# Optimization experiments

Measured on AMD Instinct MI355X. Metric: run time of the kernel, lower is better.

The kernel has to match this reference:

```python
import jax, jax.numpy as jnp
import numpy as np

H, W = 72, 128            # raster_h, raster_w
THICK = 0.03              # raster_thickness
SHARP = 80.0              # sigmoid sharpness
NRS = 64                  # match_resample_n
BIG = 1e9                 # finite stand-in for inf (grad-safe)
PTS_W, TAN_W, CURV_W, OVL_W = 5.0, 1.0, 0.5, 2.0


def _grid_xy():
    ys = jnp.linspace(0.0, 1.0, H)
    xs = jnp.linspace(0.0, 1.0, W)
    yy, xx = jnp.meshgrid(ys, xs, indexing='ij')
    return jnp.stack([xx, yy], -1).reshape(-1, 2)  # [H*W, 2]


def _prepare_mask(vis):
    # visibility -> per-point mask; curves with <2 visible points fall back to all-visible
    raw = vis > 0.5
    fallback = raw.sum(-1) < 2
    return jnp.where(fallback[:, None], 1.0, raw.astype(jnp.float32))  # [m, p]


def _resample(curves, pm, num):
    # arc-length resampling of [m, p, 2] polylines to [m, num, 2]
    m, p, _ = curves.shape
    seg_valid = pm[:, :-1] * pm[:, 1:]
    seg_len = jnp.linalg.norm(curves[:, 1:] - curves[:, :-1], axis=-1) * seg_valid
    cum = jnp.concatenate([jnp.zeros((m, 1), curves.dtype), jnp.cumsum(seg_len, -1)], -1)  # [m, p]
    total = cum[:, -1]
    base_t = jnp.linspace(0.0, 1.0, num)
    t = base_t[None] * total[:, None]  # [m, num]
    idx = jax.vmap(lambda c, tt: jnp.searchsorted(c, tt, side='right'))(cum, t) - 1
    idx = jnp.clip(idx, 0, p - 2)
    left = jnp.take_along_axis(curves[:, :-1], idx[..., None], axis=1)
    right = jnp.take_along_axis(curves[:, 1:], idx[..., None], axis=1)
    lt = jnp.take_along_axis(cum[:, :-1], idx, axis=1)
    rt = jnp.take_along_axis(cum[:, 1:], idx, axis=1)
    alpha = ((t - lt) / jnp.maximum(rt - lt, 1e-8))[..., None]
    out = left + alpha * (right - left)
    return jnp.where((total < 1e-8)[:, None, None], curves[:, :1, :], out)


def _tangents(pts):
    # central-difference unit tangents, [m, n, 2]
    fwd = jnp.concatenate([pts[:, 1:2] - pts[:, 0:1],
                           pts[:, 2:] - pts[:, :-2],
                           pts[:, -1:] - pts[:, -2:-1]], axis=1)
    return fwd / jnp.maximum(jnp.linalg.norm(fwd, axis=-1, keepdims=True), 1e-8)


def _pt2poly(A, B):
    # mean over resampled points of A of min point-to-segment distance to polyline B
    # A: [qa, r, 2], B: [qb, r, 2] -> [qa, qb]
    seg_a = B[:, :-1]
    ab = B[:, 1:] - seg_a
    denom = jnp.maximum((ab * ab).sum(-1), 1e-8)  # [qb, s]
    ap = A[:, None, :, None, :] - seg_a[None, :, None]           # [qa, qb, r, s, 2]
    t = jnp.clip((ap * ab[None, :, None]).sum(-1) / denom[None, :, None], 0.0, 1.0)
    proj = seg_a[None, :, None] + t[..., None] * ab[None, :, None]
    dist = jnp.linalg.norm(A[:, None, :, None, :] - proj, axis=-1)  # [qa, qb, r, s]
    return dist.min(-1).mean(-1)


def _smooth_l1(x, y):
    d = jnp.abs(x - y)
    return jnp.where(d < 1.0, 0.5 * d * d, d - 0.5)


def _soft_mask(curves, pm, grid):
    # soft rasterization of polylines: [m, p, 2] -> [m, H*W]
    seg_a = curves[:, :-1]
    ab = curves[:, 1:] - seg_a
    denom = jnp.maximum((ab * ab).sum(-1), 1e-8)          # [m, s]
    seg_valid = (pm[:, :-1] * pm[:, 1:]) > 0.5
    ap = grid[None, :, None, :] - seg_a[:, None]          # [m, HW, s, 2]
    t = jnp.clip((ap * ab[:, None]).sum(-1) / denom[:, None], 0.0, 1.0)
    proj = seg_a[:, None] + t[..., None] * ab[:, None]
    dist = jnp.linalg.norm(grid[None, :, None, :] - proj, axis=-1)  # [m, HW, s]
    dist = jnp.where(seg_valid[:, None], dist, BIG)
    min_dist = dist.min(-1)
    # fallback to nearest visible point when a curve has no valid segment
    no_valid = ~seg_valid.any(-1)
    pd = jnp.linalg.norm(grid[None, :, None, :] - curves[:, None], axis=-1)  # [m, HW, p]
    pd = jnp.where(pm[:, None] > 0.5, pd, BIG)
    min_dist = jnp.where(no_valid[:, None], pd.min(-1), min_dist)
    return jax.nn.sigmoid((THICK - min_dist) * SHARP)


def _cost_single(pred, gtp, gtv, grid):
    gt_pm = _prepare_mask(gtv)
    ones_pm = jnp.ones(pred.shape[:2], pred.dtype)
    pred_rs = _resample(pred, ones_pm, NRS)
    gt_rs = _resample(gtp, gt_pm, NRS)
    d_pg = _pt2poly(pred_rs, gt_rs)
    d_gp = _pt2poly(gt_rs, pred_rs).T
    sym = 0.5 * (d_pg + d_gp)                                   # [Q, M]
    pt = _tangents(pred_rs)
    gt_t = _tangents(gt_rs)
    tan = 1.0 - jnp.abs((pt[:, None] * gt_t[None]).sum(-1)).mean(-1)
    ps = pred_rs[:, 2:] - 2 * pred_rs[:, 1:-1] + pred_rs[:, :-2]
    gs = gt_rs[:, 2:] - 2 * gt_rs[:, 1:-1] + gt_rs[:, :-2]
    curv = _smooth_l1(ps[:, None], gs[None]).mean((-1, -2))
    pmask = _soft_mask(pred, ones_pm, grid)                     # [Q, HW]
    gmask = _soft_mask(gtp, gt_pm, grid)                        # [M, HW]
    inter = jnp.minimum(pmask[:, None], gmask[None]).sum(-1)
    union = jnp.maximum(pmask[:, None], gmask[None]).sum(-1)
    overlap = 1.0 - inter / (union + 1e-8)
    return PTS_W * sym + TAN_W * tan + CURV_W * curv + OVL_W * overlap


def setup_inputs() -> dict:
    key = jax.random.key(0)
    k1, k2, k3, k4 = jax.random.split(key, 4)
    return {
        'pred_pts': jax.random.uniform(k1, (2, 40, 24, 2), jnp.float32),
        'gt_pts': jax.random.uniform(k2, (2, 24, 24, 2), jnp.float32),
        'gt_vis': jax.random.uniform(k3, (2, 24, 24), jnp.float32),
        'gt_exist': jax.random.uniform(k4, (2, 24), jnp.float32),
    }


def reference(pred_pts, gt_pts, gt_vis, gt_exist):
    grid = _grid_xy()
    cost = jax.vmap(lambda p, g, v: _cost_single(p, g, v, grid))(pred_pts, gt_pts, gt_vis)
    # zero out columns for non-existent GT lanes (original skips them via boolean indexing)
    return cost * (gt_exist > 0.5).astype(cost.dtype)[:, None, :]  # [B, Q, M]
```

## Files before the change

### kernel.cpp

```cpp
#include <hip/hip_runtime.h>
#include <math.h>

#define Hh 72
#define Ww 128
#define HW (Hh*Ww)
#define NP 24
#define Mp 40
#define Ng 24
#define Bb 2
#define NRS 64
#define THICKc 0.03f
#define SHARPc 80.0f

__global__ __launch_bounds__(64) void k_resample(
    const float* __restrict__ pred,
    const float* __restrict__ gt,
    const float* __restrict__ vis,
    float* __restrict__ predRS,
    float* __restrict__ gtRS,
    float* __restrict__ gtPM)
{
    int blk = blockIdx.x;
    int b = blk / (Mp + Ng);
    int c = blk % (Mp + Ng);
    bool isPred = (c < Mp);
    int tid = threadIdx.x;

    __shared__ float qx[NP], qy[NP], pm[NP], cum[NP];
    __shared__ float s_total;

    const float* src = isPred ? pred + (size_t)(b * Mp + c) * NP * 2
                              : gt   + (size_t)(b * Ng + (c - Mp)) * NP * 2;
    if (tid < NP) {
        qx[tid] = src[tid * 2 + 0];
        qy[tid] = src[tid * 2 + 1];
        pm[tid] = isPred ? 1.0f
                         : ((vis[(b * Ng + (c - Mp)) * NP + tid] > 0.5f) ? 1.0f : 0.0f);
    }
    __syncthreads();
    if (tid == 0) {
        if (!isPred) {
            float s = 0.0f;
            for (int p = 0; p < NP; p++) s += pm[p];
            if (s < 2.0f)
                for (int p = 0; p < NP; p++) pm[p] = 1.0f;
        }
        float acc = 0.0f;
        cum[0] = 0.0f;
        for (int s = 0; s < NP - 1; s++) {
            float dx = qx[s + 1] - qx[s], dy = qy[s + 1] - qy[s];
            float sl = sqrtf(dx * dx + dy * dy) * (pm[s] * pm[s + 1]);
            acc += sl;
            cum[s + 1] = acc;
        }
        s_total = acc;
    }
    __syncthreads();
    if (!isPred && tid < NP) gtPM[(b * Ng + (c - Mp)) * NP + tid] = pm[tid];

    float total = s_total;
    float t = ((float)tid / 63.0f) * total;
    int cnt = 0;
    for (int p = 0; p < NP; p++) cnt += (cum[p] <= t) ? 1 : 0;
    int idx = cnt - 1;
    idx = (idx < 0) ? 0 : ((idx > NP - 2) ? NP - 2 : idx);
    float lt = cum[idx], rt = cum[idx + 1];
    float alpha = (t - lt) / fmaxf(rt - lt, 1e-8f);
    float ox = qx[idx] + alpha * (qx[idx + 1] - qx[idx]);
    float oy = qy[idx] + alpha * (qy[idx + 1] - qy[idx]);
    if (total < 1e-8f) { ox = qx[0]; oy = qy[0]; }
    float* dst = isPred ? predRS + (size_t)(b * Mp + c) * NRS * 2
                        : gtRS   + (size_t)(b * Ng + (c - Mp)) * NRS * 2;
    dst[tid * 2 + 0] = ox;
    dst[tid * 2 + 1] = oy;
}

__global__ __launch_bounds__(256) void k_softmask(
    const float* __restrict__ pred,
    const float* __restrict__ gt,
    const float* __restrict__ gtPM,
    float* __restrict__ pmask,
    float* __restrict__ gmask)
{
    int c = blockIdx.y;
    int b = c / (Mp + Ng);
    int cc = c % (Mp + Ng);
    bool isPred = (cc < Mp);
    int g = blockIdx.x * blockDim.x + threadIdx.x;

    __shared__ float qx[NP], qy[NP], pm[NP];
    if (threadIdx.x < NP) {
        const float* src = isPred ? pred + (size_t)(b * Mp + cc) * NP * 2
                                  : gt   + (size_t)(b * Ng + (cc - Mp)) * NP * 2;
        qx[threadIdx.x] = src[threadIdx.x * 2 + 0];
        qy[threadIdx.x] = src[threadIdx.x * 2 + 1];
        pm[threadIdx.x] = isPred ? 1.0f : gtPM[(b * Ng + (cc - Mp)) * NP + threadIdx.x];
    }
    __syncthreads();

    float gx = (float)(g % Ww) * (1.0f / 127.0f);
    float gy = (float)(g / Ww) * (1.0f / 71.0f);

    float best2 = 1e30f;
    bool anyValid = false;
    for (int s = 0; s < NP - 1; s++) {
        if (pm[s] * pm[s + 1] > 0.5f) {
            anyValid = true;
            float ax = qx[s], ay = qy[s];
            float abx = qx[s + 1] - ax, aby = qy[s + 1] - ay;
            float denom = fmaxf(abx * abx + aby * aby, 1e-8f);
            float t = ((gx - ax) * abx + (gy - ay) * aby) / denom;
            t = fminf(fmaxf(t, 0.0f), 1.0f);
            float dx = gx - (ax + t * abx), dy = gy - (ay + t * aby);
            best2 = fminf(best2, dx * dx + dy * dy);
        }
    }
    float mind;
    if (anyValid) {
        mind = sqrtf(best2);
    } else {
        float b2 = 1e30f;
        for (int p = 0; p < NP; p++) {
            if (pm[p] > 0.5f) {
                float dx = gx - qx[p], dy = gy - qy[p];
                b2 = fminf(b2, dx * dx + dy * dy);
            }
        }
        mind = sqrtf(b2);
    }
    float x = (THICKc - mind) * SHARPc;
    float mval = 1.0f / (1.0f + expf(-x));
    if (isPred) pmask[(size_t)(b * Mp + cc) * HW + g] = mval;
    else        gmask[(size_t)(b * Ng + (cc - Mp)) * HW + g] = mval;
}

__device__ __forceinline__ float block_reduce_sum(float v, float* red, int tid) {
    red[tid] = v;
    __syncthreads();
    for (int s = 128; s > 0; s >>= 1) {
        if (tid < s) red[tid] += red[tid + s];
        __syncthreads();
    }
    float r = red[0];
    __syncthreads();
    return r;
}

__global__ __launch_bounds__(256) void k_cost(
    const float* __restrict__ predRS,
    const float* __restrict__ gtRS,
    const float* __restrict__ pmask,
    const float* __restrict__ gmask,
    const float* __restrict__ gtExist,
    float* __restrict__ out)
{
    int pair = blockIdx.x;
    int j = pair % Ng;
    int i = (pair / Ng) % Mp;
    int b = pair / (Ng * Mp);
    int tid = threadIdx.x;

    __shared__ float px[NRS], py[NRS], gxr[NRS], gyr[NRS];
    __shared__ float red[256];

    if (tid < NRS) {
        px[tid]  = predRS[((size_t)(b * Mp + i) * NRS + tid) * 2 + 0];
        py[tid]  = predRS[((size_t)(b * Mp + i) * NRS + tid) * 2 + 1];
        gxr[tid] = gtRS[((size_t)(b * Ng + j) * NRS + tid) * 2 + 0];
        gyr[tid] = gtRS[((size_t)(b * Ng + j) * NRS + tid) * 2 + 1];
    }
    __syncthreads();

    const float* pmk = pmask + (size_t)(b * Mp + i) * HW;
    const float* gmk = gmask + (size_t)(b * Ng + j) * HW;
    float smin = 0.0f, smax = 0.0f;
    for (int g = tid; g < HW; g += 256) {
        float p = pmk[g], q = gmk[g];
        smin += fminf(p, q);
        smax += fmaxf(p, q);
    }

    float symv = 0.0f, tanv = 0.0f, curvv = 0.0f;
    if (tid < NRS) {
        float p0x = px[tid], p0y = py[tid];
        float bst = 1e30f;
        for (int s = 0; s < NRS - 1; s++) {
            float ax = gxr[s], ay = gyr[s];
            float abx = gxr[s + 1] - ax, aby = gyr[s + 1] - ay;
            float denom = fmaxf(abx * abx + aby * aby, 1e-8f);
            float t = ((p0x - ax) * abx + (p0y - ay) * aby) / denom;
            t = fminf(fmaxf(t, 0.0f), 1.0f);
            float dx = p0x - (ax + t * abx), dy = p0y - (ay + t * aby);
            bst = fminf(bst, dx * dx + dy * dy);
        }
        float dpg = sqrtf(bst);
        float q0x = gxr[tid], q0y = gyr[tid];
        bst = 1e30f;
        for (int s = 0; s < NRS - 1; s++) {
            float ax = px[s], ay = py[s];
            float abx = px[s + 1] - ax, aby = py[s + 1] - ay;
            float denom = fmaxf(abx * abx + aby * aby, 1e-8f);
            float t = ((q0x - ax) * abx + (q0y - ay) * aby) / denom;
            t = fminf(fmaxf(t, 0.0f), 1.0f);
            float dx = q0x - (ax + t * abx), dy = q0y - (ay + t * aby);
            bst = fminf(bst, dx * dx + dy * dy);
        }
        float dgp = sqrtf(bst);
        symv = 0.5f * (dpg + dgp);

        int kp = (tid == NRS - 1) ? NRS - 1 : tid + 1;
        int km = (tid == 0) ? 0 : tid - 1;
        float tx = px[kp] - px[km], ty = py[kp] - py[km];
        float nrm = fmaxf(sqrtf(tx * tx + ty * ty), 1e-8f);
        tx /= nrm; ty /= nrm;
        float gtx = gxr[kp] - gxr[km], gty = gyr[kp] - gyr[km];
        float nrm2 = fmaxf(sqrtf(gtx * gtx + gty * gty), 1e-8f);
        gtx /= nrm2; gty /= nrm2;
        tanv = fabsf(tx * gtx + ty * gty);

        if (tid < NRS - 2) {
            float psx = px[tid + 2] - 2.0f * px[tid + 1] + px[tid];
            float psy = py[tid + 2] - 2.0f * py[tid + 1] + py[tid];
            float gsx = gxr[tid + 2] - 2.0f * gxr[tid + 1] + gxr[tid];
            float gsy = gyr[tid + 2] - 2.0f * gyr[tid + 1] + gyr[tid];
            float d1 = fabsf(psx - gsx);
            float d2 = fabsf(psy - gsy);
            float c1 = (d1 < 1.0f) ? 0.5f * d1 * d1 : d1 - 0.5f;
            float c2 = (d2 < 1.0f) ? 0.5f * d2 * d2 : d2 - 0.5f;
            curvv = c1 + c2;
        }
    }

    float Smin  = block_reduce_sum(smin,  red, tid);
    float Smax  = block_reduce_sum(smax,  red, tid);
    float Ssym  = block_reduce_sum(symv,  red, tid);
    float Stan  = block_reduce_sum(tanv,  red, tid);
    float Scurv = block_reduce_sum(curvv, red, tid);

    if (tid == 0) {
        float overlap = 1.0f - Smin / (Smax + 1e-8f);
        float sym  = Ssym * (1.0f / 64.0f);
        float tanl = 1.0f - Stan * (1.0f / 64.0f);
        float curv = Scurv * (1.0f / 124.0f);
        float cost = 5.0f * sym + 1.0f * tanl + 0.5f * curv + 2.0f * overlap;
        float e = (gtExist[b * Ng + j] > 0.5f) ? 1.0f : 0.0f;
        out[(size_t)(b * Mp + i) * Ng + j] = cost * e;
    }
}

extern "C" void kernel_launch(void* const* d_in, const int* in_sizes, int n_in,
                              void* d_out, int out_size, void* d_ws, size_t ws_size,
                              hipStream_t stream) {
    (void)in_sizes; (void)n_in; (void)out_size; (void)ws_size;
    const float* pred  = (const float*)d_in[0];
    const float* gt    = (const float*)d_in[1];
    const float* vis   = (const float*)d_in[2];
    const float* exist = (const float*)d_in[3];

    float* ws     = (float*)d_ws;
    float* predRS = ws;
    float* gtRS   = predRS + (size_t)Bb * Mp * NRS * 2;
    float* gtPM   = gtRS   + (size_t)Bb * Ng * NRS * 2;
    float* pmask  = gtPM   + (size_t)Bb * Ng * NP;
    float* gmask  = pmask  + (size_t)Bb * Mp * HW;
    float* outp   = (float*)d_out;

    hipLaunchKernelGGL(k_resample, dim3(Bb * (Mp + Ng)), dim3(64), 0, stream,
                       pred, gt, vis, predRS, gtRS, gtPM);
    hipLaunchKernelGGL(k_softmask, dim3(HW / 256, Bb * (Mp + Ng)), dim3(256), 0, stream,
                       pred, gt, gtPM, pmask, gmask);
    hipLaunchKernelGGL(k_cost, dim3(Bb * Mp * Ng), dim3(256), 0, stream,
                       predRS, gtRS, pmask, gmask, exist, outp);
}
```

Measured before the change: 115.8 us.

## Derive mask union from per-mask sums and use wave-shuffle reductions

The soft-mask kernel now accumulates a per-mask total with a wave shuffle and an atomicAdd into a small buffer that the resample kernel zeroes. The cost kernel then gets the union sum as sum(p)+sum(q)-sum(min) and only computes the min term, reading through float4 loads. The five shared-memory tree reductions, each with many barriers, become wave shuffles plus one barrier. __expf and bit ops replace expf and div/mod. The cost is atomics in the mask kernel and slightly different float rounding in the union sum.

Result: slower. 167.2 us (+44.4%).

```diff
diff --git a/kernel.cpp b/kernel.cpp
--- a/kernel.cpp
+++ b/kernel.cpp
@@ -11,6 +11,7 @@
 #define NRS 64
 #define THICKc 0.03f
 #define SHARPc 80.0f
+#define NSUM (Bb*(Mp+Ng))
 
 __global__ __launch_bounds__(64) void k_resample(
     const float* __restrict__ pred,
@@ -18,13 +19,16 @@
     const float* __restrict__ vis,
     float* __restrict__ predRS,
     float* __restrict__ gtRS,
-    float* __restrict__ gtPM)
+    float* __restrict__ gtPM,
+    float* __restrict__ maskSum)
 {
     int blk = blockIdx.x;
     int b = blk / (Mp + Ng);
     int c = blk % (Mp + Ng);
     bool isPred = (c < Mp);
     int tid = threadIdx.x;
+
+    if (tid == 0) maskSum[blk] = 0.0f;
 
     __shared__ float qx[NP], qy[NP], pm[NP], cum[NP];
     __shared__ float s_total;
@@ -80,7 +84,8 @@
     const float* __restrict__ gt,
     const float* __restrict__ gtPM,
     float* __restrict__ pmask,
-    float* __restrict__ gmask)
+    float* __restrict__ gmask,
+    float* __restrict__ maskSum)
 {
     int c = blockIdx.y;
     int b = c / (Mp + Ng);
@@ -98,8 +103,8 @@
     }
     __syncthreads();
 
-    float gx = (float)(g % Ww) * (1.0f / 127.0f);
-    float gy = (float)(g / Ww) * (1.0f / 71.0f);
+    float gx = (float)(g & (Ww - 1)) * (1.0f / 127.0f);
+    float gy = (float)(g >> 7) * (1.0f / 71.0f);
 
     float best2 = 1e30f;
     bool anyValid = false;
@@ -129,21 +134,18 @@
         mind = sqrtf(b2);
     }
     float x = (THICKc - mind) * SHARPc;
-    float mval = 1.0f / (1.0f + expf(-x));
-    if (isPred) pmask[(size_t)(b * Mp + cc) * HW + g] = mval;
-    else        gmask[(size_t)(b * Ng + (cc - Mp)) * HW + g] = mval;
-}
-
-__device__ __forceinline__ float block_reduce_sum(float v, float* red, int tid) {
-    red[tid] = v;
-    __syncthreads();
-    for (int s = 128; s > 0; s >>= 1) {
-        if (tid < s) red[tid] += red[tid + s];
-        __syncthreads();
-    }
-    float r = red[0];
-    __syncthreads();
-    return r;
+    float mval = 1.0f / (1.0f + __expf(-x));
+    int sumIdx;
+    if (isPred) {
+        pmask[(size_t)(b * Mp + cc) * HW + g] = mval;
+        sumIdx = b * Mp + cc;
+    } else {
+        gmask[(size_t)(b * Ng + (cc - Mp)) * HW + g] = mval;
+        sumIdx = Bb * Mp + b * Ng + (cc - Mp);
+    }
+    float ws = mval;
+    for (int off = 32; off > 0; off >>= 1) ws += __shfl_down(ws, off);
+    if ((threadIdx.x & 63) == 0) atomicAdd(&maskSum[sumIdx], ws);
 }
 
 __global__ __launch_bounds__(256) void k_cost(
@@ -151,6 +153,7 @@
     const float* __restrict__ gtRS,
     const float* __restrict__ pmask,
     const float* __restrict__ gmask,
+    const float* __restrict__ maskSum,
     const float* __restrict__ gtExist,
     float* __restrict__ out)
 {
@@ -159,9 +162,10 @@
     int i = (pair / Ng) % Mp;
     int b = pair / (Ng * Mp);
     int tid = threadIdx.x;
+    int lane = tid & 63, wid = tid >> 6;
 
     __shared__ float px[NRS], py[NRS], gxr[NRS], gyr[NRS];
-    __shared__ float red[256];
+    __shared__ float partial[4];
 
     if (tid < NRS) {
         px[tid]  = predRS[((size_t)(b * Mp + i) * NRS + tid) * 2 + 0];
@@ -171,18 +175,17 @@
     }
     __syncthreads();
 
-    const float* pmk = pmask + (size_t)(b * Mp + i) * HW;
-    const float* gmk = gmask + (size_t)(b * Ng + j) * HW;
-    float smin = 0.0f, smax = 0.0f;
-    for (int g = tid; g < HW; g += 256) {
-        float p = pmk[g], q = gmk[g];
-        smin += fminf(p, q);
-        smax += fmaxf(p, q);
+    const float4* pm4 = (const float4*)(pmask + (size_t)(b * Mp + i) * HW);
+    const float4* gm4 = (const float4*)(gmask + (size_t)(b * Ng + j) * HW);
+    float smin = 0.0f;
+    for (int g = tid; g < HW / 4; g += 256) {
+        float4 p = pm4[g], q = gm4[g];
+        smin += fminf(p.x, q.x) + fminf(p.y, q.y) + fminf(p.z, q.z) + fminf(p.w, q.w);
     }
 
     float symv = 0.0f, tanv = 0.0f, curvv = 0.0f;
-    if (tid < NRS) {
-        float p0x = px[tid], p0y = py[tid];
+    if (wid == 0) {
+        float p0x = px[lane], p0y = py[lane];
         float bst = 1e30f;
         for (int s = 0; s < NRS - 1; s++) {
             float ax = gxr[s], ay = gyr[s];
@@ -194,7 +197,7 @@
             bst = fminf(bst, dx * dx + dy * dy);
         }
         float dpg = sqrtf(bst);
-        float q0x = gxr[tid], q0y = gyr[tid];
+        float q0x = gxr[lane], q0y = gyr[lane];
         bst = 1e30f;
         for (int s = 0; s < NRS - 1; s++) {
             float ax = px[s], ay = py[s];
@@ -208,8 +211,8 @@
         float dgp = sqrtf(bst);
         symv = 0.5f * (dpg + dgp);
 
-        int kp = (tid == NRS - 1) ? NRS - 1 : tid + 1;
-        int km = (tid == 0) ? 0 : tid - 1;
+        int kp = (lane == NRS - 1) ? NRS - 1 : lane + 1;
+        int km = (lane == 0) ? 0 : lane - 1;
         float tx = px[kp] - px[km], ty = py[kp] - py[km];
         float nrm = fmaxf(sqrtf(tx * tx + ty * ty), 1e-8f);
         tx /= nrm; ty /= nrm;
@@ -218,11 +221,11 @@
         gtx /= nrm2; gty /= nrm2;
         tanv = fabsf(tx * gtx + ty * gty);
 
-        if (tid < NRS - 2) {
-            float psx = px[tid + 2] - 2.0f * px[tid + 1] + px[tid];
-            float psy = py[tid + 2] - 2.0f * py[tid + 1] + py[tid];
-            float gsx = gxr[tid + 2] - 2.0f * gxr[tid + 1] + gxr[tid];
-            float gsy = gyr[tid + 2] - 2.0f * gyr[tid + 1] + gyr[tid];
+        if (lane < NRS - 2) {
+            float psx = px[lane + 2] - 2.0f * px[lane + 1] + px[lane];
+            float psy = py[lane + 2] - 2.0f * py[lane + 1] + py[lane];
+            float gsx = gxr[lane + 2] - 2.0f * gxr[lane + 1] + gxr[lane];
+            float gsy = gyr[lane + 2] - 2.0f * gyr[lane + 1] + gyr[lane];
             float d1 = fabsf(psx - gsx);
             float d2 = fabsf(psy - gsy);
             float c1 = (d1 < 1.0f) ? 0.5f * d1 * d1 : d1 - 0.5f;
@@ -231,17 +234,26 @@
         }
     }
 
-    float Smin  = block_reduce_sum(smin,  red, tid);
-    float Smax  = block_reduce_sum(smax,  red, tid);
-    float Ssym  = block_reduce_sum(symv,  red, tid);
-    float Stan  = block_reduce_sum(tanv,  red, tid);
-    float Scurv = block_reduce_sum(curvv, red, tid);
+    for (int off = 32; off > 0; off >>= 1) smin += __shfl_down(smin, off);
+    if (lane == 0) partial[wid] = smin;
+    if (wid == 0) {
+        for (int off = 32; off > 0; off >>= 1) {
+            symv  += __shfl_down(symv,  off);
+            tanv  += __shfl_down(tanv,  off);
+            curvv += __shfl_down(curvv, off);
+        }
+    }
+    __syncthreads();
 
     if (tid == 0) {
+        float Smin = partial[0] + partial[1] + partial[2] + partial[3];
+        float Sp = maskSum[b * Mp + i];
+        float Sq = maskSum[Bb * Mp + b * Ng + j];
+        float Smax = Sp + Sq - Smin;
         float overlap = 1.0f - Smin / (Smax + 1e-8f);
-        float sym  = Ssym * (1.0f / 64.0f);
-        float tanl = 1.0f - Stan * (1.0f / 64.0f);
-        float curv = Scurv * (1.0f / 124.0f);
+        float sym  = symv * (1.0f / 64.0f);
+        float tanl = 1.0f - tanv * (1.0f / 64.0f);
+        float curv = curvv * (1.0f / 124.0f);
         float cost = 5.0f * sym + 1.0f * tanl + 0.5f * curv + 2.0f * overlap;
         float e = (gtExist[b * Ng + j] > 0.5f) ? 1.0f : 0.0f;
         out[(size_t)(b * Mp + i) * Ng + j] = cost * e;
@@ -257,18 +269,19 @@
     const float* vis   = (const float*)d_in[2];
     const float* exist = (const float*)d_in[3];
 
-    float* ws     = (float*)d_ws;
-    float* predRS = ws;
-    float* gtRS   = predRS + (size_t)Bb * Mp * NRS * 2;
-    float* gtPM   = gtRS   + (size_t)Bb * Ng * NRS * 2;
-    float* pmask  = gtPM   + (size_t)Bb * Ng * NP;
-    float* gmask  = pmask  + (size_t)Bb * Mp * HW;
-    float* outp   = (float*)d_out;
+    float* ws      = (float*)d_ws;
+    float* predRS  = ws;
+    float* gtRS    = predRS + (size_t)Bb * Mp * NRS * 2;
+    float* gtPM    = gtRS   + (size_t)Bb * Ng * NRS * 2;
+    float* maskSum = gtPM   + (size_t)Bb * Ng * NP;
+    float* pmask   = maskSum + NSUM;
+    float* gmask   = pmask  + (size_t)Bb * Mp * HW;
+    float* outp    = (float*)d_out;
 
     hipLaunchKernelGGL(k_resample, dim3(Bb * (Mp + Ng)), dim3(64), 0, stream,
-                       pred, gt, vis, predRS, gtRS, gtPM);
+                       pred, gt, vis, predRS, gtRS, gtPM, maskSum);
     hipLaunchKernelGGL(k_softmask, dim3(HW / 256, Bb * (Mp + Ng)), dim3(256), 0, stream,
-                       pred, gt, gtPM, pmask, gmask);
+                       pred, gt, gtPM, pmask, gmask, maskSum);
     hipLaunchKernelGGL(k_cost, dim3(Bb * Mp * Ng), dim3(256), 0, stream,
-                       predRS, gtRS, pmask, gmask, exist, outp);
-}
+                       predRS, gtRS, pmask, gmask, maskSum, exist, outp);
+}
```
